# Kernel optimization log

Hardware: AMD Instinct MI355X
Metric: run time of the kernel (lower is better)

Reference implementation:

```python
import jax, jax.numpy as jnp
import numpy as np

EPS = 1e-5  # BatchNorm eps

B, LMAX = 64, 512
N_IN, N_OUT = 128, 256
LENGTHS = np.array([128 if i % 2 == 0 else 384 for i in range(B)], dtype=np.int64)  # sum = 16384
M = int(LENGTHS.sum())


def _bn(x, gamma, beta, mean, var):
    # eval-mode BatchNorm over channel (last) dim; x: [M, C]
    return (x - mean) * (gamma / jnp.sqrt(var + EPS)) + beta


def _aggregate(x, ld, am):
    # x: [M, N] ragged-concatenated node features; ld: [B] lengths; am: [B, L, L]
    # Equivalent to per-graph am[j,:l,:l] @ x_block, vectorized via zero-padding:
    # padded columns of am hit zero rows of x, and garbage rows are never gathered.
    Bn, L, _ = am.shape
    gid = jnp.repeat(jnp.arange(Bn), ld, total_repeat_length=x.shape[0])      # [M] graph id per node
    offs = jnp.concatenate([jnp.zeros((1,), ld.dtype), jnp.cumsum(ld)[:-1]])  # [B] start offsets
    pos = jnp.arange(x.shape[0]) - offs[gid]                                   # [M] within-graph position
    padded = jnp.zeros((Bn, L, x.shape[1]), x.dtype).at[gid, pos].set(x)       # [B, L, N]
    out = jnp.einsum('blm,bmn->bln', am, padded)                               # batched adjacency matmul
    return out[gid, pos]                                                       # back to ragged [M, N]


def setup_inputs() -> dict:
    key = jax.random.key(0)
    ks = jax.random.split(key, 12)
    x = jax.random.normal(ks[0], (M, N_IN, 1, 1), dtype=jnp.float32)
    ld = jnp.asarray(LENGTHS)
    am = jax.random.normal(ks[1], (B, LMAX, LMAX), dtype=jnp.float32)

    def lin_bn(kw, kb, cin, cout):
        W = jax.random.normal(kw, (cout, cin), dtype=jnp.float32) / np.sqrt(cin)
        b = jax.random.normal(kb, (cout,), dtype=jnp.float32) * 0.01
        kg, kbt, km, kv = jax.random.split(jax.random.fold_in(kw, 7), 4)
        gamma = 1.0 + 0.1 * jax.random.normal(kg, (cout,), dtype=jnp.float32)
        beta = 0.1 * jax.random.normal(kbt, (cout,), dtype=jnp.float32)
        mean = 0.1 * jax.random.normal(km, (cout,), dtype=jnp.float32)
        var = 0.5 + jax.random.uniform(kv, (cout,), dtype=jnp.float32)
        return W, b, gamma, beta, mean, var

    Wl, bl, gl, betal, ml, vl = lin_bn(ks[2], ks[3], N_IN, N_OUT)   # residual 1x1 conv + BN
    W1, b1, g1, beta1, m1, v1 = lin_bn(ks[4], ks[5], N_IN, N_IN)    # graph conv layer 1
    W2, b2, g2, beta2, m2, v2 = lin_bn(ks[6], ks[7], N_IN, N_OUT)   # graph conv layer 2
    return {
        'x': x, 'ld': ld, 'am': am,
        'Wl': Wl, 'bl': bl, 'gl': gl, 'betal': betal, 'ml': ml, 'vl': vl,
        'W1': W1, 'b1': b1, 'g1': g1, 'beta1': beta1, 'm1': m1, 'v1': v1,
        'W2': W2, 'b2': b2, 'g2': g2, 'beta2': beta2, 'm2': m2, 'v2': v2,
    }


def reference(x, ld, am,
              Wl, bl, gl, betal, ml, vl,
              W1, b1, g1, beta1, m1, v1,
              W2, b2, g2, beta2, m2, v2):
    xf = x.reshape(x.shape[0], x.shape[1])  # squeeze [M, N, 1, 1] -> [M, N]
    # residual branch (input_size != output_size): 1x1 conv + BN
    residual = _bn(xf @ Wl.T + bl, gl, betal, ml, vl)
    # graph conv layer 1: aggregate -> conv1x1 -> BN -> ReLU (dropout inactive in eval)
    h = _aggregate(xf, ld, am)
    h = jax.nn.relu(_bn(h @ W1.T + b1, g1, beta1, m1, v1))
    # graph conv layer 2: aggregate -> conv1x1 -> BN
    h = _aggregate(h, ld, am)
    h = _bn(h @ W2.T + b2, g2, beta2, m2, v2)
    out = jax.nn.leaky_relu(h + residual, negative_slope=0.01)
    return out[:, :, None, None]  # [M, N_out, 1, 1]
```

## Files before the change

### kernel.cpp

```cpp
#include <hip/hip_runtime.h>

#define EPS 1e-5f

typedef __attribute__((ext_vector_type(4))) float f32x4;
typedef __attribute__((ext_vector_type(8))) _Float16 f16x8;
typedef __attribute__((ext_vector_type(4))) _Float16 f16x4;

__device__ __forceinline__ int tidx(int r, int k, int K) {
    return (r >> 4) * (K << 4) + ((k >> 5) << 9) + ((r & 15) << 5) + (((k & 31) >> 3) << 3) + (k & 7);
}

#define MFMA16(a, b, c) __builtin_amdgcn_mfma_f32_16x16x32_f16(a, b, c, 0, 0, 0)

__device__ __forceinline__ void slot_map(int s, int& g, int& r0) {
    int c = s >> 6, j = s & 63;
    if (j < 48) { g = c * 8 + 2 * (j / 12) + 1; r0 = (j % 12) << 5; }
    else        { int jj = j - 48; g = c * 8 + 2 * (jj / 4); r0 = (jj % 4) << 5; }
}

__global__ __launch_bounds__(256) void prep_conv_kernel(
    const int* __restrict__ ld, const float* __restrict__ am,
    const float* __restrict__ Wl, const float* __restrict__ bl,
    const float* __restrict__ gl, const float* __restrict__ betal,
    const float* __restrict__ ml, const float* __restrict__ vl,
    const float* __restrict__ W1, const float* __restrict__ b1,
    const float* __restrict__ g1, const float* __restrict__ beta1,
    const float* __restrict__ m1, const float* __restrict__ v1,
    const float* __restrict__ W2, const float* __restrict__ b2,
    const float* __restrict__ g2, const float* __restrict__ beta2,
    const float* __restrict__ m2, const float* __restrict__ v2,
    int* __restrict__ offs, float* __restrict__ c1, float* __restrict__ cf,
    int* __restrict__ tg, int* __restrict__ tr, int* __restrict__ ta, int n_tasks,
    _Float16* __restrict__ W1t, _Float16* __restrict__ Wct,
    _Float16* __restrict__ amt,
    const float* __restrict__ x, _Float16* __restrict__ XTt,
    _Float16* __restrict__ xh_t, int M)
{
    __shared__ __align__(16) _Float16 Tt[128][80];
    int t = threadIdx.x;
    if (blockIdx.x < 256) {
        int m0 = blockIdx.x * 64;
        int gg = 0, off = 0;
        while (m0 >= off + ld[gg]) { off += ld[gg]; ++gg; }
        int l = ld[gg];
        #pragma unroll
        for (int p = 0; p < 8; ++p) {
            int idx = t + p * 256;
            int m = idx >> 5;
            int f = (idx & 31) * 4;
            float4 v = *(const float4*)&x[(size_t)(m0 + m) * 128 + f];
            Tt[f + 0][m] = (_Float16)v.x; Tt[f + 1][m] = (_Float16)v.y;
            Tt[f + 2][m] = (_Float16)v.z; Tt[f + 3][m] = (_Float16)v.w;
            f16x4 h;
            h[0] = (_Float16)v.x; h[1] = (_Float16)v.y;
            h[2] = (_Float16)v.z; h[3] = (_Float16)v.w;
            *(f16x4*)&xh_t[tidx(m0 + m, f, 128)] = h;
        }
        __syncthreads();
        #pragma unroll
        for (int p = 0; p < 4; ++p) {
            int idx = t + p * 256;
            int f = idx >> 3;
            int m8 = (idx & 7) * 8;
            int kl = m0 - off + m8;
            uint4 v = *(const uint4*)&Tt[f][m8];
            *(uint4*)&XTt[off * 128 + tidx(f, kl, l)] = v;
        }
    } else if (blockIdx.x < 320) {
        int b = blockIdx.x - 256;
        int gt = b * 256 + t;
        const int gsize = 64 * 256;
        if (b == 0) {
            if (t < 64) {
                int s = 0;
                for (int i = 0; i < t; ++i) s += ld[i];
                offs[t] = s;
            }
            if (t < 128) {
                float s1 = g1[t] * rsqrtf(v1[t] + EPS);
                c1[t] = (b1[t] - m1[t]) * s1 + beta1[t];
            }
            if (t < 256) {
                float s2 = g2[t] * rsqrtf(v2[t] + EPS);
                float sl = gl[t] * rsqrtf(vl[t] + EPS);
                cf[t] = (b2[t] - m2[t]) * s2 + beta2[t] + (bl[t] - ml[t]) * sl + betal[t];
            }
            for (int s = t; s < n_tasks; s += 256) {
                int g, r0;
                slot_map(s, g, r0);
                int amo = 0;
                for (int gg2 = 0; gg2 < g; ++gg2) { int L = ld[gg2]; amo += L * L; }
                tg[s] = g;
                tr[s] = r0;
                ta[s] = amo;
            }
        }
        for (int idx = gt; idx < 128 * 128; idx += gsize) {
            int n = idx >> 7, k = idx & 127;
            float s1 = g1[n] * rsqrtf(v1[n] + EPS);
            W1t[tidx(n, k, 128)] = (_Float16)(W1[idx] * s1);
        }
        for (int idx = gt; idx < 256 * 256; idx += gsize) {
            int n = idx >> 8, k = idx & 255;
            float v;
            if (k < 128) {
                float s2 = g2[n] * rsqrtf(v2[n] + EPS);
                v = W2[n * 128 + k] * s2;
            } else {
                float sl = gl[n] * rsqrtf(vl[n] + EPS);
                v = Wl[n * 128 + (k - 128)] * sl;
            }
            Wct[tidx(n, k, 256)] = (_Float16)v;
        }
    } else {
        int b2 = blockIdx.x - 320;
        int s = ((b2 & 7) << 6) + (b2 >> 3);
        int g, r0;
        slot_map(s, g, r0);
        int amo = 0;
        for (int gg2 = 0; gg2 < g; ++gg2) { int L = ld[gg2]; amo += L * L; }
        int l = ld[g];
        const float* src = am + (size_t)g * (512 * 512);
        _Float16* dst = amt + amo;
        int lq = l >> 2;
        int tot = lq << 5;
        for (int q = t; q < tot; q += 256) {
            int row = q / lq;
            int c4 = (q - row * lq) << 2;
            float4 v = *(const float4*)&src[(size_t)(r0 + row) * 512 + c4];
            f16x4 h;
            h[0] = (_Float16)v.x; h[1] = (_Float16)v.y;
            h[2] = (_Float16)v.z; h[3] = (_Float16)v.w;
            *(f16x4*)&dst[tidx(r0 + row, c4, l)] = h;
        }
    }
}

#define STAGED_A()                                                            \
    {                                                                         \
        uint4 cur_a = *(const uint4*)(sa);                                    \
        uint4 cur_b; if (isB) cur_b = *(const uint4*)(sb);                    \
        uint4 nxt_a = *(const uint4*)(sa + 512);                              \
        uint4 nxt_b; if (isB) nxt_b = *(const uint4*)(sb + 512);              \
        *(uint4*)&Ast[0][dstA] = cur_a;                                       \
        if (isB) *(uint4*)&Bst[0][dstB] = cur_b;                              \
        __syncthreads();                                                      \
        for (int s = 0; s < nk; s += 2) {                                     \
            uint4 fa, fb;                                                     \
            if (s + 2 < nk) {                                                 \
                fa = *(const uint4*)(sa + ((s + 2) << 9));                    \
                if (isB) fb = *(const uint4*)(sb + ((s + 2) << 9));           \
            }                                                                 \
            {                                                                 \
                f16x8 a  = *(const f16x8*)&Ast[0][(w << 9) + rdo];            \
                f16x8 b0 = *(const f16x8*)&Bst[0][rdo];                       \
                f16x8 b1 = *(const f16x8*)&Bst[0][512 + rdo];                 \
                acc0 = MFMA16(a, b0, acc0);                                   \
                acc1 = MFMA16(a, b1, acc1);                                   \
            }                                                                 \
            *(uint4*)&Ast[1][dstA] = nxt_a;                                   \
            if (isB) *(uint4*)&Bst[1][dstB] = nxt_b;                          \
            __syncthreads();                                                  \
            if (s + 3 < nk) {                                                 \
                nxt_a = *(const uint4*)(sa + ((s + 3) << 9));                 \
                if (isB) nxt_b = *(const uint4*)(sb + ((s + 3) << 9));        \
            }                                                                 \
            {                                                                 \
                f16x8 a  = *(const f16x8*)&Ast[1][(w << 9) + rdo];            \
                f16x8 b0 = *(const f16x8*)&Bst[1][rdo];                       \
                f16x8 b1 = *(const f16x8*)&Bst[1][512 + rdo];                 \
                acc0 = MFMA16(a, b0, acc0);                                   \
                acc1 = MFMA16(a, b1, acc1);                                   \
            }                                                                 \
            if (s + 2 < nk) {                                                 \
                *(uint4*)&Ast[0][dstA] = fa;                                  \
                if (isB) *(uint4*)&Bst[0][dstB] = fb;                         \
                __syncthreads();                                              \
            }                                                                 \
        }                                                                     \
    }

__global__ __launch_bounds__(512) void fused1s_kernel(
    const _Float16* __restrict__ amt, const _Float16* __restrict__ XTt,
    const int* __restrict__ ld, const int* __restrict__ offs,
    const int* __restrict__ tg, const int* __restrict__ tr, const int* __restrict__ ta,
    const _Float16* __restrict__ W1t, const float* __restrict__ bias,
    _Float16* __restrict__ H2Tt)
{
    int task = ((blockIdx.x & 7) << 6) + (blockIdx.x >> 3);
    int g = tg[task];
    int l = ld[g];
    int off = offs[g];

    int tid = threadIdx.x;
    int lane = tid & 63;
    int w = tid >> 6;
    int l15 = lane & 15;
    int l4 = lane >> 4;

    __shared__ __align__(16) _Float16 Ast[2][4096];
    __shared__ __align__(16) _Float16 Bst[2][1024];
    __shared__ __align__(16) _Float16 Hs[32][136];

    const int ts = l << 4;
    const int nk = l >> 5;
    const int lane_off = (l15 << 5) + (l4 << 3);
    const int rdo = lane_off ^ ((l15 & 7) << 3);

    int idx63 = tid & 63;
    int wr = idx63 >> 2, wc = idx63 & 3;
    int wt = (wr << 5) + (wc << 3);
    int wts = wt ^ ((wr & 7) << 3);
    const int dstA = ((tid >> 6) << 9) + wts;
    const int dstB = (((tid >> 6) & 1) << 9) + wts;
    const bool isB = tid < 128;

    const _Float16* sa = XTt + off * 128 + (tid >> 6) * ts + (idx63 << 3);
    const _Float16* sb = amt + ta[task]
        + ((tr[task] >> 4) + ((tid >> 6) & 1)) * ts + (idx63 << 3);

    f32x4 acc0 = {0.f, 0.f, 0.f, 0.f}, acc1 = acc0;
    STAGED_A()

    {
        f16x4 o0, o1;
        #pragma unroll
        for (int r = 0; r < 4; ++r) { o0[r] = (_Float16)acc0[r]; o1[r] = (_Float16)acc1[r]; }
        *(f16x4*)&Hs[l15][w * 16 + (l4 << 2)] = o0;
        *(f16x4*)&Hs[16 + l15][w * 16 + (l4 << 2)] = o1;
    }
    __syncthreads();

    const _Float16* wbase = W1t + w * 2048 + lane_off;
    f32x4 e0 = {0.f, 0.f, 0.f, 0.f}, e1 = e0;
    #pragma unroll
    for (int s = 0; s < 4; ++s) {
        int ho = (s << 5) + (l4 << 3);
        f16x8 a0 = *(const f16x8*)&Hs[l15][ho];
        f16x8 a1 = *(const f16x8*)&Hs[16 + l15][ho];
        f16x8 b  = *(const f16x8*)(wbase + (s << 9));
        e0 = MFMA16(a0, b, e0);
        e1 = MFMA16(a1, b, e1);
    }
    int hb = off * 128;
    int trb = tr[task];
    int n = w * 16 + l15;
    float bv = bias[n];
    {
        f16x4 o;
        #pragma unroll
        for (int r = 0; r < 4; ++r) {
            float v = e0[r] + bv;
            o[r] = (_Float16)(v > 0.f ? v : 0.f);
        }
        *(f16x4*)&H2Tt[hb + tidx(n, trb + (l4 << 2), l)] = o;
    }
    {
        f16x4 o;
        #pragma unroll
        for (int r = 0; r < 4; ++r) {
            float v = e1[r] + bv;
            o[r] = (_Float16)(v > 0.f ? v : 0.f);
        }
        *(f16x4*)&H2Tt[hb + tidx(n, trb + 16 + (l4 << 2), l)] = o;
    }
}

__global__ __launch_bounds__(512) void fused2s_kernel(
    const _Float16* __restrict__ amt, const _Float16* __restrict__ H2Tt,
    const int* __restrict__ ld, const int* __restrict__ offs,
    const int* __restrict__ tg, const int* __restrict__ tr, const int* __restrict__ ta,
    const _Float16* __restrict__ xh_t, const _Float16* __restrict__ Wct,
    const float* __restrict__ bias, float* __restrict__ out)
{
    int task = ((blockIdx.x & 7) << 6) + (blockIdx.x >> 3);
    int g = tg[task];
    int l = ld[g];
    int off = offs[g];

    int tid = threadIdx.x;
    int lane = tid & 63;
    int w = tid >> 6;
    int l15 = lane & 15;
    int l4 = lane >> 4;

    __shared__ __align__(16) _Float16 Ast[2][4096];
    __shared__ __align__(16) _Float16 Bst[2][1024];
    __shared__ __align__(16) _Float16 Hs[32][136];

    const int ts = l << 4;
    const int nk = l >> 5;
    const int lane_off = (l15 << 5) + (l4 << 3);
    const int rdo = lane_off ^ ((l15 & 7) << 3);

    int idx63 = tid & 63;
    int wr = idx63 >> 2, wc = idx63 & 3;
    int wt = (wr << 5) + (wc << 3);
    int wts = wt ^ ((wr & 7) << 3);
    const int dstA = ((tid >> 6) << 9) + wts;
    const int dstB = (((tid >> 6) & 1) << 9) + wts;
    const bool isB = tid < 128;

    const _Float16* sa = H2Tt + off * 128 + (tid >> 6) * ts + (idx63 << 3);
    const _Float16* sb = amt + ta[task]
        + ((tr[task] >> 4) + ((tid >> 6) & 1)) * ts + (idx63 << 3);

    f32x4 acc0 = {0.f, 0.f, 0.f, 0.f}, acc1 = acc0;
    STAGED_A()

    {
        f16x4 o0, o1;
        #pragma unroll
        for (int r = 0; r < 4; ++r) { o0[r] = (_Float16)acc0[r]; o1[r] = (_Float16)acc1[r]; }
        *(f16x4*)&Hs[l15][w * 16 + (l4 << 2)] = o0;
        *(f16x4*)&Hs[16 + l15][w * 16 + (l4 << 2)] = o1;
    }
    __syncthreads();

    int gmb = off + tr[task];
    const _Float16* wb0 = Wct + (w * 2) * 4096 + lane_off;
    const _Float16* wb1 = wb0 + 4096;
    const _Float16* xp0 = xh_t + (gmb >> 4) * 2048 + lane_off;
    const _Float16* xp1 = xp0 + 2048;
    f32x4 e00 = {0.f, 0.f, 0.f, 0.f}, e01 = e00, e10 = e00, e11 = e00;
    #pragma unroll
    for (int s = 0; s < 8; ++s) {
        f16x8 a0, a1;
        if (s < 4) {
            int ho = (s << 5) + (l4 << 3);
            a0 = *(const f16x8*)&Hs[l15][ho];
            a1 = *(const f16x8*)&Hs[16 + l15][ho];
        } else {
            a0 = *(const f16x8*)(xp0 + ((s - 4) << 9));
            a1 = *(const f16x8*)(xp1 + ((s - 4) << 9));
        }
        f16x8 b0 = *(const f16x8*)(wb0 + (s << 9));
        f16x8 b1 = *(const f16x8*)(wb1 + (s << 9));
        e00 = MFMA16(a0, b0, e00);
        e01 = MFMA16(a1, b0, e01);
        e10 = MFMA16(a0, b1, e10);
        e11 = MFMA16(a1, b1, e11);
    }
    int n0 = w * 32 + l15;
    int n1 = n0 + 16;
    float bv0 = bias[n0], bv1 = bias[n1];
    #pragma unroll
    for (int r = 0; r < 4; ++r) {
        int m0r = gmb + (l4 << 2) + r;
        int m1r = m0r + 16;
        float v;
        v = e00[r] + bv0; out[(size_t)m0r * 256 + n0] = v > 0.f ? v : 0.01f * v;
        v = e01[r] + bv0; out[(size_t)m1r * 256 + n0] = v > 0.f ? v : 0.01f * v;
        v = e10[r] + bv1; out[(size_t)m0r * 256 + n1] = v > 0.f ? v : 0.01f * v;
        v = e11[r] + bv1; out[(size_t)m1r * 256 + n1] = v > 0.f ? v : 0.01f * v;
    }
}

extern "C" void kernel_launch(void* const* d_in, const int* in_sizes, int n_in,
                              void* d_out, int out_size, void* d_ws, size_t ws_size,
                              hipStream_t stream) {
    const float* x     = (const float*)d_in[0];
    const int*   ld    = (const int*)d_in[1];
    const float* am    = (const float*)d_in[2];
    const float* Wl    = (const float*)d_in[3];
    const float* bl    = (const float*)d_in[4];
    const float* gl    = (const float*)d_in[5];
    const float* betal = (const float*)d_in[6];
    const float* ml    = (const float*)d_in[7];
    const float* vl    = (const float*)d_in[8];
    const float* W1    = (const float*)d_in[9];
    const float* b1    = (const float*)d_in[10];
    const float* g1    = (const float*)d_in[11];
    const float* beta1 = (const float*)d_in[12];
    const float* m1    = (const float*)d_in[13];
    const float* v1    = (const float*)d_in[14];
    const float* W2    = (const float*)d_in[15];
    const float* b2    = (const float*)d_in[16];
    const float* g2    = (const float*)d_in[17];
    const float* beta2 = (const float*)d_in[18];
    const float* m2    = (const float*)d_in[19];
    const float* v2    = (const float*)d_in[20];
    float* out = (float*)d_out;

    int M = in_sizes[0] / 128;
    int n_tasks = M / 32;

    char* w = (char*)d_ws;
    int*   offs = (int*)(w);
    float* c1   = (float*)(w + 512);
    float* cf   = (float*)(w + 1024);
    int*   tg   = (int*)(w + 2048);
    int*   tr   = (int*)(w + 4096);
    int*   ta   = (int*)(w + 6144);
    _Float16* W1t = (_Float16*)(w + 16384);
    _Float16* Wct = (_Float16*)(w + 49152);
    _Float16* amt = (_Float16*)(w + 180224);
    _Float16* XTt = (_Float16*)(w + 180224 + (size_t)10485760);
    _Float16* xh_t = XTt + (size_t)M * 128;
    _Float16* H2Tt = xh_t + (size_t)M * 128;

    prep_conv_kernel<<<832, 256, 0, stream>>>(ld, am,
        Wl, bl, gl, betal, ml, vl,
        W1, b1, g1, beta1, m1, v1,
        W2, b2, g2, beta2, m2, v2,
        offs, c1, cf, tg, tr, ta, n_tasks, W1t, Wct, amt, x, XTt, xh_t, M);

    fused1s_kernel<<<n_tasks, 512, 0, stream>>>(amt, XTt, ld, offs, tg, tr, ta, W1t, c1, H2Tt);

    fused2s_kernel<<<n_tasks, 512, 0, stream>>>(amt, H2Tt, ld, offs, tg, tr, ta, xh_t, Wct, cf, out);
}
```

Before: 38.96 us.

## Fuse adjacency fp16 conversion into first aggregation kernel

Removes the separate adjacency-tile conversion blocks from the prep kernel. The first fused aggregation kernel now reads the fp32 adjacency directly, converts it to fp16 in registers, stages it into shared memory for the MFMA loop, and writes the tiled fp16 copy for the second layer. This drops one global round trip of the converted adjacency and shrinks the prep launch. In exchange the first kernel's B loads double in bytes and gain conversion work on its critical path.

```diff
diff --git a/kernel.cpp b/kernel.cpp
--- a/kernel.cpp
+++ b/kernel.cpp
@@ -11,6 +11,13 @@
 }
 
 #define MFMA16(a, b, c) __builtin_amdgcn_mfma_f32_16x16x32_f16(a, b, c, 0, 0, 0)
+
+__device__ __forceinline__ f16x8 cvt8(float4 a, float4 b) {
+    f16x8 h;
+    h[0] = (_Float16)a.x; h[1] = (_Float16)a.y; h[2] = (_Float16)a.z; h[3] = (_Float16)a.w;
+    h[4] = (_Float16)b.x; h[5] = (_Float16)b.y; h[6] = (_Float16)b.z; h[7] = (_Float16)b.w;
+    return h;
+}
 
 __device__ __forceinline__ void slot_map(int s, int& g, int& r0) {
     int c = s >> 6, j = s & 63;
@@ -19,7 +26,7 @@
 }
 
 __global__ __launch_bounds__(256) void prep_conv_kernel(
-    const int* __restrict__ ld, const float* __restrict__ am,
+    const int* __restrict__ ld,
     const float* __restrict__ Wl, const float* __restrict__ bl,
     const float* __restrict__ gl, const float* __restrict__ betal,
     const float* __restrict__ ml, const float* __restrict__ vl,
@@ -32,7 +39,6 @@
     int* __restrict__ offs, float* __restrict__ c1, float* __restrict__ cf,
     int* __restrict__ tg, int* __restrict__ tr, int* __restrict__ ta, int n_tasks,
     _Float16* __restrict__ W1t, _Float16* __restrict__ Wct,
-    _Float16* __restrict__ amt,
     const float* __restrict__ x, _Float16* __restrict__ XTt,
     _Float16* __restrict__ xh_t, int M)
 {
@@ -66,7 +72,7 @@
             uint4 v = *(const uint4*)&Tt[f][m8];
             *(uint4*)&XTt[off * 128 + tidx(f, kl, l)] = v;
         }
-    } else if (blockIdx.x < 320) {
+    } else {
         int b = blockIdx.x - 256;
         int gt = b * 256 + t;
         const int gsize = 64 * 256;
@@ -112,27 +118,154 @@
             }
             Wct[tidx(n, k, 256)] = (_Float16)v;
         }
-    } else {
-        int b2 = blockIdx.x - 320;
-        int s = ((b2 & 7) << 6) + (b2 >> 3);
-        int g, r0;
-        slot_map(s, g, r0);
-        int amo = 0;
-        for (int gg2 = 0; gg2 < g; ++gg2) { int L = ld[gg2]; amo += L * L; }
-        int l = ld[g];
-        const float* src = am + (size_t)g * (512 * 512);
-        _Float16* dst = amt + amo;
-        int lq = l >> 2;
-        int tot = lq << 5;
-        for (int q = t; q < tot; q += 256) {
-            int row = q / lq;
-            int c4 = (q - row * lq) << 2;
-            float4 v = *(const float4*)&src[(size_t)(r0 + row) * 512 + c4];
-            f16x4 h;
-            h[0] = (_Float16)v.x; h[1] = (_Float16)v.y;
-            h[2] = (_Float16)v.z; h[3] = (_Float16)v.w;
-            *(f16x4*)&dst[tidx(r0 + row, c4, l)] = h;
-        }
+    }
+}
+
+__global__ __launch_bounds__(512) void fused1s_kernel(
+    const float* __restrict__ am, const _Float16* __restrict__ XTt,
+    const int* __restrict__ ld, const int* __restrict__ offs,
+    const int* __restrict__ tg, const int* __restrict__ tr, const int* __restrict__ ta,
+    const _Float16* __restrict__ W1t, const float* __restrict__ bias,
+    _Float16* __restrict__ amt, _Float16* __restrict__ H2Tt)
+{
+    int task = ((blockIdx.x & 7) << 6) + (blockIdx.x >> 3);
+    int g = tg[task];
+    int l = ld[g];
+    int off = offs[g];
+
+    int tid = threadIdx.x;
+    int lane = tid & 63;
+    int w = tid >> 6;
+    int l15 = lane & 15;
+    int l4 = lane >> 4;
+
+    __shared__ __align__(16) _Float16 Ast[2][4096];
+    __shared__ __align__(16) _Float16 Bst[2][1024];
+    __shared__ __align__(16) _Float16 Hs[32][136];
+
+    const int ts = l << 4;
+    const int nk = l >> 5;
+    const int lane_off = (l15 << 5) + (l4 << 3);
+    const int rdo = lane_off ^ ((l15 & 7) << 3);
+
+    int idx63 = tid & 63;
+    int wr = idx63 >> 2, wc = idx63 & 3;
+    int wt = (wr << 5) + (wc << 3);
+    int wts = wt ^ ((wr & 7) << 3);
+    const int dstA = ((tid >> 6) << 9) + wts;
+    const int dstB = (((tid >> 6) & 1) << 9) + wts;
+    const bool isB = tid < 128;
+
+    const _Float16* sa = XTt + off * 128 + (tid >> 6) * ts + (idx63 << 3);
+    const float* sbf = am + (size_t)g * 262144
+        + (size_t)(tr[task] + (((tid >> 6) & 1) << 4) + wr) * 512 + (wc << 3);
+    _Float16* sbw = amt + ta[task]
+        + ((tr[task] >> 4) + ((tid >> 6) & 1)) * ts + wt;
+
+    f32x4 acc0 = {0.f, 0.f, 0.f, 0.f}, acc1 = acc0;
+    {
+        uint4 cur_a = *(const uint4*)(sa);
+        float4 cb0, cb1, nb0, nb1;
+        if (isB) { cb0 = *(const float4*)(sbf); cb1 = *(const float4*)(sbf + 4); }
+        uint4 nxt_a = *(const uint4*)(sa + 512);
+        if (isB) { nb0 = *(const float4*)(sbf + 32); nb1 = *(const float4*)(sbf + 36); }
+        *(uint4*)&Ast[0][dstA] = cur_a;
+        if (isB) {
+            f16x8 hb = cvt8(cb0, cb1);
+            *(f16x8*)&Bst[0][dstB] = hb;
+            *(f16x8*)(sbw) = hb;
+        }
+        __syncthreads();
+        for (int s = 0; s < nk; s += 2) {
+            uint4 fa; float4 fb0, fb1;
+            if (s + 2 < nk) {
+                fa = *(const uint4*)(sa + ((s + 2) << 9));
+                if (isB) {
+                    fb0 = *(const float4*)(sbf + ((s + 2) << 5));
+                    fb1 = *(const float4*)(sbf + ((s + 2) << 5) + 4);
+                }
+            }
+            {
+                f16x8 a  = *(const f16x8*)&Ast[0][(w << 9) + rdo];
+                f16x8 b0 = *(const f16x8*)&Bst[0][rdo];
+                f16x8 b1 = *(const f16x8*)&Bst[0][512 + rdo];
+                acc0 = MFMA16(a, b0, acc0);
+                acc1 = MFMA16(a, b1, acc1);
+            }
+            *(uint4*)&Ast[1][dstA] = nxt_a;
+            if (isB) {
+                f16x8 hb = cvt8(nb0, nb1);
+                *(f16x8*)&Bst[1][dstB] = hb;
+                *(f16x8*)(sbw + ((s + 1) << 9)) = hb;
+            }
+            __syncthreads();
+            if (s + 3 < nk) {
+                nxt_a = *(const uint4*)(sa + ((s + 3) << 9));
+                if (isB) {
+                    nb0 = *(const float4*)(sbf + ((s + 3) << 5));
+                    nb1 = *(const float4*)(sbf + ((s + 3) << 5) + 4);
+                }
+            }
+            {
+                f16x8 a  = *(const f16x8*)&Ast[1][(w << 9) + rdo];
+                f16x8 b0 = *(const f16x8*)&Bst[1][rdo];
+                f16x8 b1 = *(const f16x8*)&Bst[1][512 + rdo];
+                acc0 = MFMA16(a, b0, acc0);
+                acc1 = MFMA16(a, b1, acc1);
+            }
+            if (s + 2 < nk) {
+                *(uint4*)&Ast[0][dstA] = fa;
+                if (isB) {
+                    f16x8 hb = cvt8(fb0, fb1);
+                    *(f16x8*)&Bst[0][dstB] = hb;
+                    *(f16x8*)(sbw + ((s + 2) << 9)) = hb;
+                }
+                __syncthreads();
+            }
+        }
+    }
+
+    {
+        f16x4 o0, o1;
+        #pragma unroll
+        for (int r = 0; r < 4; ++r) { o0[r] = (_Float16)acc0[r]; o1[r] = (_Float16)acc1[r]; }
+        *(f16x4*)&Hs[l15][w * 16 + (l4 << 2)] = o0;
+        *(f16x4*)&Hs[16 + l15][w * 16 + (l4 << 2)] = o1;
+    }
+    __syncthreads();
+
+    const _Float16* wbase = W1t + w * 2048 + lane_off;
+    f32x4 e0 = {0.f, 0.f, 0.f, 0.f}, e1 = e0;
+    #pragma unroll
+    for (int s = 0; s < 4; ++s) {
+        int ho = (s << 5) + (l4 << 3);
+        f16x8 a0 = *(const f16x8*)&Hs[l15][ho];
+        f16x8 a1 = *(const f16x8*)&Hs[16 + l15][ho];
+        f16x8 b  = *(const f16x8*)(wbase + (s << 9));
+        e0 = MFMA16(a0, b, e0);
+        e1 = MFMA16(a1, b, e1);
+    }
+    int hb = off * 128;
+    int trb = tr[task];
+    int n = w * 16 + l15;
+    float bv = bias[n];
+    {
+        f16x4 o;
+        #pragma unroll
+        for (int r = 0; r < 4; ++r) {
+            float v = e0[r] + bv;
+            o[r] = (_Float16)(v > 0.f ? v : 0.f);
+        }
+        *(f16x4*)&H2Tt[hb + tidx(n, trb + (l4 << 2), l)] = o;
+    }
+    {
+        f16x4 o;
+        #pragma unroll
+        for (int r = 0; r < 4; ++r) {
+            float v = e1[r] + bv;
+            o[r] = (_Float16)(v > 0.f ? v : 0.f);
+        }
+        *(f16x4*)&H2Tt[hb + tidx(n, trb + 16 + (l4 << 2), l)] = o;
     }
 }
 
@@ -180,92 +313,6 @@
         }                                                                     \
     }
 
-__global__ __launch_bounds__(512) void fused1s_kernel(
-    const _Float16* __restrict__ amt, const _Float16* __restrict__ XTt,
-    const int* __restrict__ ld, const int* __restrict__ offs,
-    const int* __restrict__ tg, const int* __restrict__ tr, const int* __restrict__ ta,
-    const _Float16* __restrict__ W1t, const float* __restrict__ bias,
-    _Float16* __restrict__ H2Tt)
-{
-    int task = ((blockIdx.x & 7) << 6) + (blockIdx.x >> 3);
-    int g = tg[task];
-    int l = ld[g];
-    int off = offs[g];
-
-    int tid = threadIdx.x;
-    int lane = tid & 63;
-    int w = tid >> 6;
-    int l15 = lane & 15;
-    int l4 = lane >> 4;
-
-    __shared__ __align__(16) _Float16 Ast[2][4096];
-    __shared__ __align__(16) _Float16 Bst[2][1024];
-    __shared__ __align__(16) _Float16 Hs[32][136];
-
-    const int ts = l << 4;
-    const int nk = l >> 5;
-    const int lane_off = (l15 << 5) + (l4 << 3);
-    const int rdo = lane_off ^ ((l15 & 7) << 3);
-
-    int idx63 = tid & 63;
-    int wr = idx63 >> 2, wc = idx63 & 3;
-    int wt = (wr << 5) + (wc << 3);
-    int wts = wt ^ ((wr & 7) << 3);
-    const int dstA = ((tid >> 6) << 9) + wts;
-    const int dstB = (((tid >> 6) & 1) << 9) + wts;
-    const bool isB = tid < 128;
-
-    const _Float16* sa = XTt + off * 128 + (tid >> 6) * ts + (idx63 << 3);
-    const _Float16* sb = amt + ta[task]
-        + ((tr[task] >> 4) + ((tid >> 6) & 1)) * ts + (idx63 << 3);
-
-    f32x4 acc0 = {0.f, 0.f, 0.f, 0.f}, acc1 = acc0;
-    STAGED_A()
-
-    {
-        f16x4 o0, o1;
-        #pragma unroll
-        for (int r = 0; r < 4; ++r) { o0[r] = (_Float16)acc0[r]; o1[r] = (_Float16)acc1[r]; }
-        *(f16x4*)&Hs[l15][w * 16 + (l4 << 2)] = o0;
-        *(f16x4*)&Hs[16 + l15][w * 16 + (l4 << 2)] = o1;
-    }
-    __syncthreads();
-
-    const _Float16* wbase = W1t + w * 2048 + lane_off;
-    f32x4 e0 = {0.f, 0.f, 0.f, 0.f}, e1 = e0;
-    #pragma unroll
-    for (int s = 0; s < 4; ++s) {
-        int ho = (s << 5) + (l4 << 3);
-        f16x8 a0 = *(const f16x8*)&Hs[l15][ho];
-        f16x8 a1 = *(const f16x8*)&Hs[16 + l15][ho];
-        f16x8 b  = *(const f16x8*)(wbase + (s << 9));
-        e0 = MFMA16(a0, b, e0);
-        e1 = MFMA16(a1, b, e1);
-    }
-    int hb = off * 128;
-    int trb = tr[task];
-    int n = w * 16 + l15;
-    float bv = bias[n];
-    {
-        f16x4 o;
-        #pragma unroll
-        for (int r = 0; r < 4; ++r) {
-            float v = e0[r] + bv;
-            o[r] = (_Float16)(v > 0.f ? v : 0.f);
-        }
-        *(f16x4*)&H2Tt[hb + tidx(n, trb + (l4 << 2), l)] = o;
-    }
-    {
-        f16x4 o;
-        #pragma unroll
-        for (int r = 0; r < 4; ++r) {
-            float v = e1[r] + bv;
-            o[r] = (_Float16)(v > 0.f ? v : 0.f);
-        }
-        *(f16x4*)&H2Tt[hb + tidx(n, trb + 16 + (l4 << 2), l)] = o;
-    }
-}
-
 __global__ __launch_bounds__(512) void fused2s_kernel(
     const _Float16* __restrict__ amt, const _Float16* __restrict__ H2Tt,
     const int* __restrict__ ld, const int* __restrict__ offs,
@@ -399,13 +446,13 @@
     _Float16* xh_t = XTt + (size_t)M * 128;
     _Float16* H2Tt = xh_t + (size_t)M * 128;
 
-    prep_conv_kernel<<<832, 256, 0, stream>>>(ld, am,
+    prep_conv_kernel<<<320, 256, 0, stream>>>(ld,
         Wl, bl, gl, betal, ml, vl,
         W1, b1, g1, beta1, m1, v1,
         W2, b2, g2, beta2, m2, v2,
-        offs, c1, cf, tg, tr, ta, n_tasks, W1t, Wct, amt, x, XTt, xh_t, M);
-
-    fused1s_kernel<<<n_tasks, 512, 0, stream>>>(amt, XTt, ld, offs, tg, tr, ta, W1t, c1, H2Tt);
+        offs, c1, cf, tg, tr, ta, n_tasks, W1t, Wct, x, XTt, xh_t, M);
+
+    fused1s_kernel<<<n_tasks, 512, 0, stream>>>(am, XTt, ld, offs, tg, tr, ta, W1t, c1, amt, H2Tt);
 
     fused2s_kernel<<<n_tasks, 512, 0, stream>>>(amt, H2Tt, ld, offs, tg, tr, ta, xh_t, Wct, cf, out);
 }
```

After: 42.30 us. +8.6%, slower.
